# Performance work log

Measured on AMD Instinct MI355X. Metric: run time of the kernel, lower is better.

Reference implementation:

```python
import jax, jax.numpy as jnp
import numpy as np


def _mlp(h, weights, biases, n_relu):
    # Linear(+ReLU) stack; ReLU on the first n_relu layers, final layer linear only.
    for i, (w, b) in enumerate(zip(weights, biases)):
        h = h @ w + b
        if i < n_relu:
            h = jax.nn.relu(h)
    return h


def setup_inputs() -> dict:
    key = jax.random.key(0)
    ks = jax.random.split(key, 12)
    B, M, E = 16384, 512, 1024

    def lin(k, fan_in, fan_out):
        # xavier-ish scaling so activations stay well-conditioned
        return jax.random.normal(k, (fan_in, fan_out), jnp.float32) * (1.0 / np.sqrt(fan_in))

    return {
        "x": jax.random.normal(ks[0], (B, M), jnp.float32),
        "rand_noise": jax.random.uniform(ks[1], (B, M), jnp.float32),
        "u_random": jax.random.uniform(ks[2], (B, M), jnp.float32),
        "marginals_min": jnp.zeros((M,), jnp.float32),
        "marginals_max": jnp.ones((M,), jnp.float32),
        "enc_w0": lin(ks[3], M, E), "enc_b0": jnp.full((E,), 0.01, jnp.float32),
        "enc_w1": lin(ks[4], E, E), "enc_b1": jnp.full((E,), 0.01, jnp.float32),
        "enc_w2": lin(ks[5], E, E), "enc_b2": jnp.full((E,), 0.01, jnp.float32),
        "enc_w3": lin(ks[6], E, E), "enc_b3": jnp.full((E,), 0.01, jnp.float32),
        "head_w0": lin(ks[7], E, E), "head_b0": jnp.full((E,), 0.01, jnp.float32),
        "head_w1": lin(ks[8], E, E), "head_b1": jnp.full((E,), 0.01, jnp.float32),
        "corruption_len": 307,
    }


def reference(x, rand_noise, u_random, marginals_min, marginals_max,
              enc_w0, enc_b0, enc_w1, enc_b1, enc_w2, enc_b2, enc_w3, enc_b3,
              head_w0, head_b0, head_w1, head_b1, corruption_len):
    B, M = x.shape
    # Vectorized equivalent of per-row randperm(m)[:corruption_len]:
    # top-k of iid uniform noise picks a uniform random subset of size k per row.
    _, idx = jax.lax.top_k(rand_noise, corruption_len)            # [B, k]
    mask = jnp.zeros((B, M), bool).at[jnp.arange(B)[:, None], idx].set(True)

    # Marginal samples ~ Uniform(min, max) per feature.
    x_random = marginals_min + u_random * (marginals_max - marginals_min)
    x_corrupted = jnp.where(mask, x_random, x)

    enc_ws = [enc_w0, enc_w1, enc_w2, enc_w3]
    enc_bs = [enc_b0, enc_b1, enc_b2, enc_b3]
    head_ws = [head_w0, head_w1]
    head_bs = [head_b0, head_b1]

    # Run both branches through one batched pass (same math, fewer launches).
    both = jnp.concatenate([x, x_corrupted], axis=0)              # [2B, M]
    h = _mlp(both, enc_ws, enc_bs, n_relu=3)                      # encoder depth 4
    h = _mlp(h, head_ws, head_bs, n_relu=1)                       # head depth 2
    embeddings, embeddings_corrupted = h[:B], h[B:]
    return embeddings, embeddings_corrupted
```

## Files before the change

kernel.cpp:

```cpp
#include <hip/hip_runtime.h>

typedef _Float16 f16x8 __attribute__((ext_vector_type(8)));
typedef float f32x4 __attribute__((ext_vector_type(4)));
typedef float f32x16 __attribute__((ext_vector_type(16)));

__device__ __forceinline__ void gload16(const void* g, void* l) {
  __builtin_amdgcn_global_load_lds(
      (const __attribute__((address_space(1))) void*)g,
      (__attribute__((address_space(3))) void*)l, 16, 0, 0);
}

__device__ __forceinline__ void barfence() {
  asm volatile("" ::: "memory");
  __builtin_amdgcn_s_barrier();
  asm volatile("" ::: "memory");
}

__device__ __forceinline__ int xcd_swz(int orig, int nwg) {
  int q = nwg >> 3, r = nwg & 7;
  int x = orig & 7, loc = orig >> 3;
  int base = (x < r) ? x * (q + 1) : r * (q + 1) + (x - r) * q;
  return base + loc;
}

struct WPtrs { const float* w[6]; _Float16* wt[6]; };
__global__ __launch_bounds__(256) void transpose_all(WPtrs p) {
  const int N = 1024;
  __shared__ float tile[32][33];
  int y = blockIdx.y, layer, ky;
  if (y < 16) { layer = 0; ky = y; }
  else { int t = y - 16; layer = 1 + (t >> 5); ky = t & 31; }
  int K = (layer == 0) ? 512 : 1024;
  const float* W = p.w[layer];
  _Float16* WT = p.wt[layer];
  int tx = threadIdx.x, ty = threadIdx.y;
  int n0 = blockIdx.x * 32, k0 = ky * 32;
#pragma unroll
  for (int i = 0; i < 4; i++)
    tile[ty + i * 8][tx] = W[(long)(k0 + ty + i * 8) * N + (n0 + tx)];
  __syncthreads();
#pragma unroll
  for (int i = 0; i < 4; i++)
    WT[(long)(n0 + ty + i * 8) * K + (k0 + tx)] = (_Float16)tile[tx][ty + i * 8];
}

__global__ __launch_bounds__(256) void cast_f16(const float* __restrict__ in,
                                                _Float16* __restrict__ out, long n) {
  long i = ((long)blockIdx.x * 256 + threadIdx.x) * 4;
  if (i < n) {
    float4 v = *(const float4*)(in + i);
    typedef _Float16 f16x4 __attribute__((ext_vector_type(4)));
    f16x4 o = {(_Float16)v.x, (_Float16)v.y, (_Float16)v.z, (_Float16)v.w};
    *(f16x4*)(out + i) = o;
  }
}

__global__ __launch_bounds__(256) void topk_corrupt(
    const float* __restrict__ noise, const float* __restrict__ x,
    const float* __restrict__ u, const float* __restrict__ mmin,
    const float* __restrict__ mmax, const int* __restrict__ kptr,
    _Float16* __restrict__ dplain, _Float16* __restrict__ dcorr,
    int xrow0, int nrows) {
  int lane = threadIdx.x & 63;
  int r = (blockIdx.x << 2) + (threadIdx.x >> 6);
  if (r >= nrows) return;
  long row = (long)xrow0 + r;
  long rb = row * 512 + lane * 8;
  float4 n0 = *(const float4*)(noise + rb);
  float4 n1 = *(const float4*)(noise + rb + 4);
  unsigned v[8] = {__float_as_uint(n0.x), __float_as_uint(n0.y),
                   __float_as_uint(n0.z), __float_as_uint(n0.w),
                   __float_as_uint(n1.x), __float_as_uint(n1.y),
                   __float_as_uint(n1.z), __float_as_uint(n1.w)};
  int kk = *kptr;
  unsigned T = 0;
  for (int bit = 30; bit >= 0; --bit) {
    unsigned Tp = T | (1u << bit);
    int c = 0;
#pragma unroll
    for (int j = 0; j < 8; j++) c += (int)__popcll(__ballot(v[j] >= Tp));
    if (c >= kk) T = Tp;
  }
  int cgt = 0;
  unsigned long long eqb[8];
#pragma unroll
  for (int j = 0; j < 8; j++) {
    cgt += (int)__popcll(__ballot(v[j] > T));
    eqb[j] = __ballot(v[j] == T);
  }
  int need = kk - cgt;
  unsigned long long below = (1ull << lane) - 1ull;
  int rank_base = 0;
#pragma unroll
  for (int j = 0; j < 8; j++) rank_base += (int)__popcll(eqb[j] & below);

  float4 x0 = *(const float4*)(x + rb);
  float4 x1 = *(const float4*)(x + rb + 4);
  float4 u0 = *(const float4*)(u + rb);
  float4 u1 = *(const float4*)(u + rb + 4);
  int col = lane * 8;
  float4 mn0 = *(const float4*)(mmin + col);
  float4 mn1 = *(const float4*)(mmin + col + 4);
  float4 mx0 = *(const float4*)(mmax + col);
  float4 mx1 = *(const float4*)(mmax + col + 4);
  float xs[8] = {x0.x, x0.y, x0.z, x0.w, x1.x, x1.y, x1.z, x1.w};
  float us[8] = {u0.x, u0.y, u0.z, u0.w, u1.x, u1.y, u1.z, u1.w};
  float mns[8] = {mn0.x, mn0.y, mn0.z, mn0.w, mn1.x, mn1.y, mn1.z, mn1.w};
  float mxs[8] = {mx0.x, mx0.y, mx0.z, mx0.w, mx1.x, mx1.y, mx1.z, mx1.w};

  f16x8 po, co;
  int loc = 0;
#pragma unroll
  for (int j = 0; j < 8; j++) {
    bool eq = (v[j] == T);
    int rank = rank_base + loc;
    bool m = (v[j] > T) || (eq && (rank < need));
    loc += eq ? 1 : 0;
    float rv = mns[j] + us[j] * (mxs[j] - mns[j]);
    float cv = m ? rv : xs[j];
    po[j] = (_Float16)xs[j];
    co[j] = (_Float16)cv;
  }
  long ob = (long)r * 512 + lane * 8;
  if (dplain) *(f16x8*)(dplain + ob) = po;
  *(f16x8*)(dcorr + ob) = co;
}

template <bool RELU, bool OUTF32>
__global__ __launch_bounds__(512, 2) void gemm8p(const _Float16* __restrict__ A,
                                                 const _Float16* __restrict__ BT,
                                                 const float* __restrict__ bias,
                                                 void* __restrict__ Cout, int K) {
  const int N = 1024;
  __shared__ _Float16 S[2][4][8192];
  int tid = threadIdx.x;
  int lane = tid & 63, wave = tid >> 6;
  int wr = wave >> 2, wc = wave & 3;
  int logical = xcd_swz(blockIdx.x, gridDim.x);
  long arow0 = (long)(logical >> 2) * 256;
  int bcol0 = (logical & 3) * 256;

  int srow = tid >> 3;
  int scg = (tid & 7) ^ (srow & 7);
  const _Float16* gA[2][2];
  const _Float16* gB[2][2];
#pragma unroll
  for (int h = 0; h < 2; h++)
#pragma unroll
    for (int j = 0; j < 2; j++) {
      gA[h][j] = A + (arow0 + h * 128 + j * 64 + srow) * (long)K + scg * 8;
      gB[h][j] = BT + (long)(bcol0 + h * 128 + j * 64 + srow) * K + scg * 8;
    }
  int lo = tid * 8;

#define STG_A(BUF, H, T)                                   \
  do {                                                     \
    gload16(gA[H][0] + (T) * 64, &S[BUF][H][lo]);          \
    gload16(gA[H][1] + (T) * 64, &S[BUF][H][4096 + lo]);   \
  } while (0)
#define STG_B(BUF, H, T)                                      \
  do {                                                        \
    gload16(gB[H][0] + (T) * 64, &S[BUF][2 + H][lo]);         \
    gload16(gB[H][1] + (T) * 64, &S[BUF][2 + H][4096 + lo]);  \
  } while (0)

  int l31 = lane & 31, hi = lane >> 5, e2 = l31 & 7;
  int acs[4];
#pragma unroll
  for (int kk = 0; kk < 4; kk++) acs[kk] = ((kk * 2 + hi) ^ e2) * 8;
  int aoff2[2];
#pragma unroll
  for (int mb = 0; mb < 2; mb++) aoff2[mb] = (wr * 64 + mb * 32 + l31) * 64;
  int boff2 = (wc * 32 + l31) * 64;

  f16x8 af[2][4];
  f16x8 bf[2][4];
  f32x16 acc[2][2][2] = {};

#define LDA(BUF, MQ)                                                 \
  do {                                                               \
    _Pragma("unroll") for (int mb = 0; mb < 2; mb++)                 \
    _Pragma("unroll") for (int kk = 0; kk < 4; kk++)                 \
      af[mb][kk] = *(const f16x8*)&S[BUF][MQ][aoff2[mb] + acs[kk]];  \
  } while (0)
#define LDB(BUF, NQ)                                                 \
  do {                                                               \
    _Pragma("unroll") for (int kk = 0; kk < 4; kk++)                 \
      bf[NQ][kk] = *(const f16x8*)&S[BUF][2 + NQ][boff2 + acs[kk]];  \
  } while (0)
#define MFMA_Q(MQ, NQ)                                               \
  do {                                                               \
    __builtin_amdgcn_s_setprio(1);                                   \
    _Pragma("unroll") for (int kk = 0; kk < 4; kk++)                 \
    _Pragma("unroll") for (int mb = 0; mb < 2; mb++)                 \
      acc[MQ][NQ][mb] = __builtin_amdgcn_mfma_f32_32x32x16_f16(      \
          af[mb][kk], bf[NQ][kk], acc[MQ][NQ][mb], 0, 0, 0);         \
    __builtin_amdgcn_s_setprio(0);                                   \
  } while (0)

  int NT = K / 64;
  STG_A(0, 0, 0); STG_B(0, 0, 0); STG_A(0, 1, 0); STG_B(0, 1, 0);
  if (NT > 1) {
    STG_A(1, 0, 1); STG_B(1, 0, 1);
    asm volatile("s_waitcnt vmcnt(4)" ::: "memory");
  } else {
    asm volatile("s_waitcnt vmcnt(0)" ::: "memory");
  }
  barfence();

  for (int t = 0; t < NT; ++t) {
    int buf = t & 1, nbuf = buf ^ 1;
    LDB(buf, 0);
    LDA(buf, 0);
    if (t + 1 < NT) { STG_A(nbuf, 1, t + 1); STG_B(nbuf, 1, t + 1); }
    MFMA_Q(0, 0);
    barfence();
    LDB(buf, 1);
    if (t + 2 < NT) STG_A(buf, 0, t + 2);
    MFMA_Q(0, 1);
    barfence();
    LDA(buf, 1);
    if (t + 2 < NT) STG_B(buf, 0, t + 2);
    MFMA_Q(1, 0);
    barfence();
    if (t + 1 < NT) {
      if (t + 2 < NT) asm volatile("s_waitcnt vmcnt(4)" ::: "memory");
      else            asm volatile("s_waitcnt vmcnt(0)" ::: "memory");
    }
    MFMA_Q(1, 1);
    if (t + 1 < NT) barfence();
  }
#undef STG_A
#undef STG_B
#undef LDA
#undef LDB
#undef MFMA_Q

  float bv2[2];
#pragma unroll
  for (int nq = 0; nq < 2; nq++) bv2[nq] = bias[bcol0 + nq * 128 + wc * 32 + l31];
#pragma unroll
  for (int mq = 0; mq < 2; mq++)
#pragma unroll
    for (int mb = 0; mb < 2; mb++) {
      long rowb = arow0 + mq * 128 + wr * 64 + mb * 32 + hi * 4;
#pragma unroll
      for (int nq = 0; nq < 2; nq++) {
        int col = bcol0 + nq * 128 + wc * 32 + l31;
#pragma unroll
        for (int rg = 0; rg < 16; rg++) {
          long rrow = rowb + (rg & 3) + 8 * (rg >> 2);
          float v = acc[mq][nq][mb][rg] + bv2[nq];
          if (RELU) v = fmaxf(v, 0.f);
          if (OUTF32) ((float*)Cout)[rrow * N + col] = v;
          else ((_Float16*)Cout)[rrow * N + col] = (_Float16)v;
        }
      }
    }
}

extern "C" void kernel_launch(void* const* d_in, const int* in_sizes, int n_in,
                              void* d_out, int out_size, void* d_ws, size_t ws_size,
                              hipStream_t stream) {
  const float* x    = (const float*)d_in[0];
  const float* rn   = (const float*)d_in[1];
  const float* ur   = (const float*)d_in[2];
  const float* mmin = (const float*)d_in[3];
  const float* mmax = (const float*)d_in[4];
  const float* W[6]  = {(const float*)d_in[5],  (const float*)d_in[7],  (const float*)d_in[9],
                        (const float*)d_in[11], (const float*)d_in[13], (const float*)d_in[15]};
  const float* Bi[6] = {(const float*)d_in[6],  (const float*)d_in[8],  (const float*)d_in[10],
                        (const float*)d_in[12], (const float*)d_in[14], (const float*)d_in[16]};
  const int* kptr = (const int*)d_in[17];
  float* out = (float*)d_out;

  const long B = 16384;
  const int E = 1024;
  const int Ks[6] = {512, 1024, 1024, 1024, 1024, 1024};

  char* ws = (char*)d_ws;
  _Float16* wT[6];
  size_t off = 0;
  for (int i = 0; i < 6; i++) { wT[i] = (_Float16*)(ws + off); off += (size_t)Ks[i] * E * 2; }
  size_t rem = (ws_size > off) ? ws_size - off : 0;
  long R = 32768;
  while (R > 256 && (size_t)R * 5120 > rem) R >>= 1;

  _Float16* bothc = (_Float16*)(ws + off);
  _Float16* h0 = bothc + R * 512;
  _Float16* h1 = h0 + R * 1024;

  WPtrs wp;
  for (int i = 0; i < 6; i++) { wp.w[i] = W[i]; wp.wt[i] = wT[i]; }
  transpose_all<<<dim3(E / 32, 16 + 5 * 32), dim3(32, 8), 0, stream>>>(wp);

  for (long r0 = 0; r0 < 2 * B; r0 += R) {
    if (R == 2 * B) {
      topk_corrupt<<<dim3((unsigned)(B / 4)), dim3(256), 0, stream>>>(
          rn, x, ur, mmin, mmax, kptr, bothc, bothc + B * 512, 0, (int)B);
    } else {
      long plainEnd = (r0 < B) ? ((r0 + R < B) ? (r0 + R) : B) : r0;
      long p1 = plainEnd - r0;
      if (p1 > 0) {
        long n = p1 * 512;
        long blocks = (n / 4 + 255) / 256;
        cast_f16<<<dim3((unsigned)blocks), dim3(256), 0, stream>>>(x + r0 * 512, bothc, n);
      }
      long c0 = (r0 > B) ? r0 : B;
      long p2 = (r0 + R) - c0;
      if (p2 > 0) {
        topk_corrupt<<<dim3((unsigned)((p2 + 3) / 4)), dim3(256), 0, stream>>>(
            rn, x, ur, mmin, mmax, kptr, (_Float16*)nullptr,
            bothc + (c0 - r0) * 512, (int)(c0 - B), (int)p2);
      }
    }
    dim3 gg((unsigned)((R / 256) * 4)), gb(512);
    gemm8p<true,  false><<<gg, gb, 0, stream>>>(bothc, wT[0], Bi[0], (void*)h0, 512);
    gemm8p<true,  false><<<gg, gb, 0, stream>>>(h0,    wT[1], Bi[1], (void*)h1, 1024);
    gemm8p<true,  false><<<gg, gb, 0, stream>>>(h1,    wT[2], Bi[2], (void*)h0, 1024);
    gemm8p<false, false><<<gg, gb, 0, stream>>>(h0,    wT[3], Bi[3], (void*)h1, 1024);
    gemm8p<true,  false><<<gg, gb, 0, stream>>>(h1,    wT[4], Bi[4], (void*)h0, 1024);
    gemm8p<false, true ><<<gg, gb, 0, stream>>>(h0,    wT[5], Bi[5],
                                                 (void*)(out + r0 * 1024), 1024);
  }
}
```

Baseline: 436.6 us.

## Use MFMA-native LDS layout and reorder pipelined GEMM stages with register double buffering

The global-to-LDS staging mapping now writes tiles directly in the per-lane MFMA fragment order, so each wave's LDS reads become linear and need no XOR swizzle. The main loop is reordered: A and B fragments are double-buffered in registers (af0/af1, bf0/bf1), the next tile's loads are issued earlier, and the quadrant MFMA order is rearranged to hide LDS and global latency. This trades more register pressure and a looser wait schedule for fewer bank conflicts and better overlap, at some risk of prefetch ordering hazards.

```diff
diff --git a/kernel.cpp b/kernel.cpp
--- a/kernel.cpp
+++ b/kernel.cpp
@@ -1,7 +1,6 @@
 #include <hip/hip_runtime.h>
 
 typedef _Float16 f16x8 __attribute__((ext_vector_type(8)));
-typedef float f32x4 __attribute__((ext_vector_type(4)));
 typedef float f32x16 __attribute__((ext_vector_type(16)));
 
 __device__ __forceinline__ void gload16(const void* g, void* l) {
@@ -140,16 +139,18 @@
   long arow0 = (long)(logical >> 2) * 256;
   int bcol0 = (logical & 3) * 256;
 
-  int srow = tid >> 3;
-  int scg = (tid & 7) ^ (srow & 7);
+  int scol = ((((tid >> 6) & 3) * 2 + ((tid >> 5) & 1))) * 8;
+  int srw[2];
+#pragma unroll
+  for (int r = 0; r < 2; r++) srw[r] = (r * 2 + (tid >> 8)) * 32 + (tid & 31);
   const _Float16* gA[2][2];
   const _Float16* gB[2][2];
 #pragma unroll
   for (int h = 0; h < 2; h++)
 #pragma unroll
-    for (int j = 0; j < 2; j++) {
-      gA[h][j] = A + (arow0 + h * 128 + j * 64 + srow) * (long)K + scg * 8;
-      gB[h][j] = BT + (long)(bcol0 + h * 128 + j * 64 + srow) * K + scg * 8;
+    for (int r = 0; r < 2; r++) {
+      gA[h][r] = A + (arow0 + h * 128 + srw[r]) * (long)K + scol;
+      gB[h][r] = BT + (long)(bcol0 + h * 128 + srw[r]) * K + scol;
     }
   int lo = tid * 8;
 
@@ -164,70 +165,57 @@
     gload16(gB[H][1] + (T) * 64, &S[BUF][2 + H][4096 + lo]);  \
   } while (0)
 
-  int l31 = lane & 31, hi = lane >> 5, e2 = l31 & 7;
-  int acs[4];
-#pragma unroll
-  for (int kk = 0; kk < 4; kk++) acs[kk] = ((kk * 2 + hi) ^ e2) * 8;
-  int aoff2[2];
-#pragma unroll
-  for (int mb = 0; mb < 2; mb++) aoff2[mb] = (wr * 64 + mb * 32 + l31) * 64;
-  int boff2 = (wc * 32 + l31) * 64;
-
-  f16x8 af[2][4];
-  f16x8 bf[2][4];
+  f16x8 af0[2][4], af1[2][4];
+  f16x8 bf0[4], bf1[4];
   f32x16 acc[2][2][2] = {};
 
-#define LDA(BUF, MQ)                                                 \
-  do {                                                               \
-    _Pragma("unroll") for (int mb = 0; mb < 2; mb++)                 \
-    _Pragma("unroll") for (int kk = 0; kk < 4; kk++)                 \
-      af[mb][kk] = *(const f16x8*)&S[BUF][MQ][aoff2[mb] + acs[kk]];  \
-  } while (0)
-#define LDB(BUF, NQ)                                                 \
-  do {                                                               \
-    _Pragma("unroll") for (int kk = 0; kk < 4; kk++)                 \
-      bf[NQ][kk] = *(const f16x8*)&S[BUF][2 + NQ][boff2 + acs[kk]];  \
-  } while (0)
-#define MFMA_Q(MQ, NQ)                                               \
+#define LDA(DST, BUF, MQ)                                                     \
+  do {                                                                        \
+    _Pragma("unroll") for (int mb = 0; mb < 2; mb++)                          \
+    _Pragma("unroll") for (int kk = 0; kk < 4; kk++)                          \
+      DST[mb][kk] =                                                           \
+          *(const f16x8*)&S[BUF][MQ][(((wr * 2 + mb) * 4 + kk) * 64 + lane) * 8]; \
+  } while (0)
+#define LDB(DST, BUF, NQ)                                                     \
+  do {                                                                        \
+    _Pragma("unroll") for (int kk = 0; kk < 4; kk++)                          \
+      DST[kk] = *(const f16x8*)&S[BUF][2 + NQ][((wc * 4 + kk) * 64 + lane) * 8]; \
+  } while (0)
+#define MFMA_Q(AF, BF, MQ, NQ)                                       \
   do {                                                               \
     __builtin_amdgcn_s_setprio(1);                                   \
     _Pragma("unroll") for (int kk = 0; kk < 4; kk++)                 \
     _Pragma("unroll") for (int mb = 0; mb < 2; mb++)                 \
       acc[MQ][NQ][mb] = __builtin_amdgcn_mfma_f32_32x32x16_f16(      \
-          af[mb][kk], bf[NQ][kk], acc[MQ][NQ][mb], 0, 0, 0);         \
+          AF[mb][kk], BF[kk], acc[MQ][NQ][mb], 0, 0, 0);             \
     __builtin_amdgcn_s_setprio(0);                                   \
   } while (0)
 
   int NT = K / 64;
-  STG_A(0, 0, 0); STG_B(0, 0, 0); STG_A(0, 1, 0); STG_B(0, 1, 0);
-  if (NT > 1) {
-    STG_A(1, 0, 1); STG_B(1, 0, 1);
-    asm volatile("s_waitcnt vmcnt(4)" ::: "memory");
-  } else {
-    asm volatile("s_waitcnt vmcnt(0)" ::: "memory");
-  }
+  STG_B(0, 0, 0); STG_B(0, 1, 0); STG_A(0, 0, 0); STG_A(0, 1, 0);
+  asm volatile("s_waitcnt vmcnt(2)" ::: "memory");
   barfence();
+  LDA(af0, 0, 0);
+  LDB(bf1, 0, 1);
 
   for (int t = 0; t < NT; ++t) {
     int buf = t & 1, nbuf = buf ^ 1;
-    LDB(buf, 0);
-    LDA(buf, 0);
-    if (t + 1 < NT) { STG_A(nbuf, 1, t + 1); STG_B(nbuf, 1, t + 1); }
-    MFMA_Q(0, 0);
+    LDB(bf0, buf, 0);
+    if (t + 1 < NT) { STG_B(nbuf, 0, t + 1); STG_B(nbuf, 1, t + 1); }
+    MFMA_Q(af0, bf0, 0, 0);
+    if (t + 1 < NT) asm volatile("s_waitcnt vmcnt(4)" ::: "memory");
+    else            asm volatile("s_waitcnt vmcnt(0)" ::: "memory");
     barfence();
-    LDB(buf, 1);
-    if (t + 2 < NT) STG_A(buf, 0, t + 2);
-    MFMA_Q(0, 1);
+    LDA(af1, buf, 1);
+    if (t + 1 < NT) STG_A(nbuf, 0, t + 1);
+    MFMA_Q(af0, bf1, 0, 1);
     barfence();
-    LDA(buf, 1);
-    if (t + 2 < NT) STG_B(buf, 0, t + 2);
-    MFMA_Q(1, 0);
+    if (t + 1 < NT) STG_A(nbuf, 1, t + 1);
+    MFMA_Q(af1, bf1, 1, 1);
+    if (t + 1 < NT) asm volatile("s_waitcnt vmcnt(2)" ::: "memory");
     barfence();
-    if (t + 1 < NT) {
-      if (t + 2 < NT) asm volatile("s_waitcnt vmcnt(4)" ::: "memory");
-      else            asm volatile("s_waitcnt vmcnt(0)" ::: "memory");
-    }
-    MFMA_Q(1, 1);
+    if (t + 1 < NT) { LDA(af0, nbuf, 0); LDB(bf1, nbuf, 1); }
+    MFMA_Q(af1, bf0, 1, 0);
     if (t + 1 < NT) barfence();
   }
 #undef STG_A
@@ -236,6 +224,7 @@
 #undef LDB
 #undef MFMA_Q
 
+  int l31 = lane & 31, hi = lane >> 5;
   float bv2[2];
 #pragma unroll
   for (int nq = 0; nq < 2; nq++) bv2[nq] = bias[bcol0 + nq * 128 + wc * 32 + l31];
```

Measured after the change: 493.7 us. 13.1% more time.
